# Performance work log

Measured on AMD Instinct MI355X. Metric: run time of the kernel, lower is better.

The kernel has to match this reference:

```python
import jax, jax.numpy as jnp
import numpy as np

IN_FEATS, N_HIDDEN, NUM_LAYERS, N_CLASSES, CLS_HIDDEN = 166, 76, 2, 2, 510
T, N, E = 3, 100000, 1600000
RRELU_SLOPE = (1.0 / 8.0 + 1.0 / 3.0) / 2.0  # eval-mode RReLU = leaky relu with mean slope


def setup_inputs() -> dict:
    key = jax.random.key(0)
    ks = jax.random.split(key, 24)
    d = {}
    d['feats'] = jax.random.normal(ks[0], (T, N, IN_FEATS), jnp.float32)
    d['src'] = jax.random.randint(ks[1], (T, E), 0, N, jnp.int32)
    d['dst'] = jax.random.randint(ks[2], (T, E), 0, N, jnp.int32)
    # TopK scorers (uniform +-1/sqrt(feats))
    s0 = 1.0 / np.sqrt(IN_FEATS)
    s1 = 1.0 / np.sqrt(N_HIDDEN)
    d['scorer0'] = jax.random.uniform(ks[3], (IN_FEATS, 1), jnp.float32, -s0, s0)
    d['scorer1'] = jax.random.uniform(ks[4], (N_HIDDEN, 1), jnp.float32, -s1, s1)
    # GCN weights (xavier-ish)
    d['gcn_w0'] = jax.random.normal(ks[5], (IN_FEATS, N_HIDDEN), jnp.float32) * np.sqrt(2.0 / (IN_FEATS + N_HIDDEN))
    d['gcn_w1'] = jax.random.normal(ks[6], (N_HIDDEN, N_HIDDEN), jnp.float32) * np.sqrt(2.0 / (2 * N_HIDDEN))
    # GRU params, torch layout: W_ih [3H, H_in], W_hh [3H, H], gate order (r, z, n)
    g = 1.0 / np.sqrt(N_HIDDEN)
    H3 = 3 * N_HIDDEN
    d['gru0_wih'] = jax.random.uniform(ks[7], (H3, N_HIDDEN), jnp.float32, -g, g)
    d['gru0_whh'] = jax.random.uniform(ks[8], (H3, N_HIDDEN), jnp.float32, -g, g)
    d['gru0_bih'] = jax.random.uniform(ks[9], (H3,), jnp.float32, -g, g)
    d['gru0_bhh'] = jax.random.uniform(ks[10], (H3,), jnp.float32, -g, g)
    d['gru1_wih'] = jax.random.uniform(ks[11], (H3, N_HIDDEN), jnp.float32, -g, g)
    d['gru1_whh'] = jax.random.uniform(ks[12], (H3, N_HIDDEN), jnp.float32, -g, g)
    d['gru1_bih'] = jax.random.uniform(ks[13], (H3,), jnp.float32, -g, g)
    d['gru1_bhh'] = jax.random.uniform(ks[14], (H3,), jnp.float32, -g, g)
    # MLP
    m1 = 1.0 / np.sqrt(N_HIDDEN)
    m2 = 1.0 / np.sqrt(CLS_HIDDEN)
    d['mlp_w1'] = jax.random.uniform(ks[15], (N_HIDDEN, CLS_HIDDEN), jnp.float32, -m1, m1)
    d['mlp_b1'] = jax.random.uniform(ks[16], (CLS_HIDDEN,), jnp.float32, -m1, m1)
    d['mlp_w2'] = jax.random.uniform(ks[17], (CLS_HIDDEN, N_CLASSES), jnp.float32, -m2, m2)
    d['mlp_b2'] = jax.random.uniform(ks[18], (N_CLASSES,), jnp.float32, -m2, m2)
    return d


def _topk_pool(x, scorer, k):
    # x: [N, F]; returns X_tilde: [F, k]
    scores = (x @ scorer).ravel() / jnp.linalg.norm(scorer)
    vals, idx = jax.lax.top_k(scores, k)
    out = x[idx] * jnp.tanh(vals)[:, None]  # [k, F]
    return out.T


def _gru_step(x, h, wih, whh, bih, bhh):
    # x: [B, H_in], h: [B, H]; torch GRU gate order r, z, n
    gx = x @ wih.T + bih
    gh = h @ whh.T + bhh
    H = h.shape[1]
    rx, zx, nx = gx[:, :H], gx[:, H:2 * H], gx[:, 2 * H:]
    rh, zh, nh = gh[:, :H], gh[:, H:2 * H], gh[:, 2 * H:]
    r = jax.nn.sigmoid(rx + rh)
    z = jax.nn.sigmoid(zx + zh)
    n = jnp.tanh(nx + r * nh)
    return (1.0 - z) * n + z * h


def _graph_conv(x, W, src, dst, n_nodes):
    # DGL GraphConv, norm='both', bias=False, RReLU (eval) activation
    deg_out = jnp.zeros((n_nodes,), x.dtype).at[src].add(1.0)
    deg_in = jnp.zeros((n_nodes,), x.dtype).at[dst].add(1.0)
    norm_src = jnp.clip(deg_out, 1.0, None) ** -0.5
    norm_dst = jnp.clip(deg_in, 1.0, None) ** -0.5
    h = (x * norm_src[:, None]) @ W  # project first (small out dim)
    agg = jax.ops.segment_sum(h[src], dst, num_segments=n_nodes)
    out = agg * norm_dst[:, None]
    return jnp.where(out >= 0, out, out * RRELU_SLOPE)


def reference(feats, src, dst, scorer0, scorer1, gcn_w0, gcn_w1,
              gru0_wih, gru0_whh, gru0_bih, gru0_bhh,
              gru1_wih, gru1_whh, gru1_bih, gru1_bhh,
              mlp_w1, mlp_b1, mlp_w2, mlp_b2):
    scorers = [scorer0, scorer1]
    gcn_ws = [gcn_w0, gcn_w1]
    grus = [(gru0_wih, gru0_whh, gru0_bih, gru0_bhh),
            (gru1_wih, gru1_whh, gru1_bih, gru1_bhh)]
    feat_list = [feats[t] for t in range(T)]
    for i in range(NUM_LAYERS):
        W = gcn_ws[i]
        wih, whh, bih, bhh = grus[i]
        for t in range(T):
            x_tilde = _topk_pool(feat_list[t], scorers[i], N_HIDDEN)  # [F, k]
            W = _gru_step(x_tilde, W, wih, whh, bih, bhh)  # evolve weights
            feat_list[t] = _graph_conv(feat_list[t], W, src[t], dst[t], N)
    h = feat_list[-1]
    h = jax.nn.relu(h @ mlp_w1 + mlp_b1)
    return h @ mlp_w2 + mlp_b2
```

## Files before the change

### kernel.cpp

```cpp
#include <hip/hip_runtime.h>
#include <math.h>

#define NN 100000
#define EE 1600000
#define F0 166
#define HID 76
#define H3 228
#define CHID 510
#define SLOPE 0.22916666666666666f
#define CAND_MAX 4096
#define NBIN 4096
#define HPAD 20

#define BSH 9
#define BSZ 512
#define NBKT 196
#define CH 4096
#define NCHK 391
#define NBAND 13

__device__ __forceinline__ unsigned f2key(float f){
    unsigned u = __float_as_uint(f);
    return (u & 0x80000000u) ? ~u : (u | 0x80000000u);
}
__device__ __forceinline__ float key2f(unsigned k){
    unsigned u = (k & 0x80000000u) ? (k & 0x7fffffffu) : ~k;
    return __uint_as_float(u);
}

__global__ void scorer_norms_k(const float* __restrict__ s0, const float* __restrict__ s1,
                               float* __restrict__ outn){
    __shared__ float red[256];
    int tid = threadIdx.x;
    float a = 0.f;
    for (int k = tid; k < F0; k += 256) a += s0[k]*s0[k];
    red[tid] = a; __syncthreads();
    for (int s = 128; s > 0; s >>= 1){ if (tid < s) red[tid] += red[tid+s]; __syncthreads(); }
    if (tid == 0) outn[0] = 1.0f/sqrtf(red[0]);
    __syncthreads();
    float b = 0.f;
    for (int k = tid; k < HID; k += 256) b += s1[k]*s1[k];
    red[tid] = b; __syncthreads();
    for (int s = 128; s > 0; s >>= 1){ if (tid < s) red[tid] += red[tid+s]; __syncthreads(); }
    if (tid == 0) outn[1] = 1.0f/sqrtf(red[0]);
}

__global__ void pad_k(const float* __restrict__ w1, const float* __restrict__ b1,
                      const float* __restrict__ w2, float* __restrict__ w1t,
                      float* __restrict__ b1p, float* __restrict__ w2p){
    int idx = blockIdx.x*256 + threadIdx.x;
    if (idx < 512*HID){
        int j = idx / HID, k = idx - j*HID;
        w1t[idx] = (j < CHID) ? w1[k*CHID + j] : 0.f;
    }
    if (idx < 512)  b1p[idx] = (idx < CHID)   ? b1[idx] : 0.f;
    if (idx < 1024) w2p[idx] = (idx < CHID*2) ? w2[idx] : 0.f;
}


__global__ __launch_bounds__(256) void p1_hist_k(const int* __restrict__ src, const int* __restrict__ dst,
                                                 int* __restrict__ bhS, int* __restrict__ bhD){
    __shared__ int hS[NBKT], hD[NBKT];
    int t = blockIdx.y, blk = blockIdx.x, tid = threadIdx.x;
    for (int i = tid; i < NBKT; i += 256){ hS[i] = 0; hD[i] = 0; }
    __syncthreads();
    size_t ebase = (size_t)t*EE + (size_t)blk*CH;
    int m = EE - blk*CH; if (m > CH) m = CH;
    for (int j = tid; j < m; j += 256){
        atomicAdd(&hS[src[ebase + j] >> BSH], 1);
        atomicAdd(&hD[dst[ebase + j] >> BSH], 1);
    }
    __syncthreads();
    for (int i = tid; i < NBKT; i += 256){
        bhS[((size_t)t*NBKT + i)*NCHK + blk] = hS[i];
        bhD[((size_t)t*NBKT + i)*NCHK + blk] = hD[i];
    }
}

__global__ __launch_bounds__(512) void p2_scan_k(int* __restrict__ bhS, int* __restrict__ bhD,
                                                 int* __restrict__ ctS, int* __restrict__ ctD){
    __shared__ int sd[512];
    int b = blockIdx.x, t = blockIdx.y, tid = threadIdx.x;
    for (int a = 0; a < 2; a++){
        int* bh = a ? bhD : bhS;
        int* ct = a ? ctD : ctS;
        int* row = bh + ((size_t)t*NBKT + b)*NCHK;
        int v = (tid < NCHK) ? row[tid] : 0;
        sd[tid] = v; __syncthreads();
        for (int off = 1; off < 512; off <<= 1){
            int x = (tid >= off) ? sd[tid - off] : 0;
            __syncthreads();
            sd[tid] += x;
            __syncthreads();
        }
        if (tid < NCHK) row[tid] = sd[tid] - v;
        if (tid == 511) ct[t*NBKT + b] = sd[511];
        __syncthreads();
    }
}

__global__ __launch_bounds__(256) void p3_base_k(const int* __restrict__ ctS, const int* __restrict__ ctD,
                                                 int* __restrict__ bbS, int* __restrict__ bbD){
    __shared__ int sd[256];
    int tid = threadIdx.x;
    for (int a = 0; a < 2; a++){
        const int* ct = a ? ctD : ctS;
        int* bb = a ? bbD : bbS;
        for (int t = 0; t < 3; t++){
            int v = (tid < NBKT) ? ct[t*NBKT + tid] : 0;
            sd[tid] = v; __syncthreads();
            for (int off = 1; off < 256; off <<= 1){
                int x = (tid >= off) ? sd[tid - off] : 0;
                __syncthreads();
                sd[tid] += x;
                __syncthreads();
            }
            if (tid < NBKT) bb[t*(NBKT+1) + tid] = sd[tid] - v;
            if (tid == 0)   bb[t*(NBKT+1) + NBKT] = EE;
            __syncthreads();
        }
    }
}

__global__ __launch_bounds__(256) void p4_scatter_k(const int* __restrict__ src, const int* __restrict__ dst,
                                                    const int* __restrict__ bhS, const int* __restrict__ bhD,
                                                    const int* __restrict__ bbS, const int* __restrict__ bbD,
                                                    int* __restrict__ srcpart,
                                                    unsigned long long* __restrict__ pairpart){
    __shared__ int baseS[NBKT], baseD[NBKT], cS[NBKT], cD[NBKT];
    int t = blockIdx.y, blk = blockIdx.x, tid = threadIdx.x;
    for (int i = tid; i < NBKT; i += 256){
        baseS[i] = bbS[t*(NBKT+1) + i] + bhS[((size_t)t*NBKT + i)*NCHK + blk];
        baseD[i] = bbD[t*(NBKT+1) + i] + bhD[((size_t)t*NBKT + i)*NCHK + blk];
        cS[i] = 0; cD[i] = 0;
    }
    __syncthreads();
    size_t ebase = (size_t)t*EE + (size_t)blk*CH;
    int m = EE - blk*CH; if (m > CH) m = CH;
    int* sp = srcpart + (size_t)t*EE;
    unsigned long long* pp = pairpart + (size_t)t*EE;
    for (int j = tid; j < m; j += 256){
        int s = src[ebase + j], d = dst[ebase + j];
        int bs = s >> BSH, bd = d >> BSH;
        int r0 = atomicAdd(&cS[bs], 1);
        sp[baseS[bs] + r0] = s;
        int r1 = atomicAdd(&cD[bd], 1);
        pp[baseD[bd] + r1] = ((unsigned long long)(unsigned)s << 32) | (unsigned)d;
    }
}

__global__ __launch_bounds__(256) void p5_degO_k(const int* __restrict__ srcpart,
                                                 const int* __restrict__ bbS,
                                                 float* __restrict__ nO){
    __shared__ int cnt[BSZ];
    int b = blockIdx.x, t = blockIdx.y, tid = threadIdx.x;
    for (int i = tid; i < BSZ; i += 256) cnt[i] = 0;
    __syncthreads();
    int st = bbS[t*(NBKT+1) + b], en = bbS[t*(NBKT+1) + b + 1];
    const int* sp = srcpart + (size_t)t*EE;
    for (int j = st + tid; j < en; j += 256) atomicAdd(&cnt[sp[j] & (BSZ-1)], 1);
    __syncthreads();
    int nb = b << BSH;
    for (int i = tid; i < BSZ; i += 256){
        int n = nb + i;
        if (n < NN){
            int o = cnt[i]; if (o < 1) o = 1;
            nO[t*NN + n] = 1.0f/sqrtf((float)o);
        }
    }
}

__global__ __launch_bounds__(512) void p6_csr_k(const unsigned long long* __restrict__ pairpart,
                                                const int* __restrict__ bbD,
                                                int* __restrict__ degI, int* __restrict__ rs,
                                                float* __restrict__ nI,
                                                int* __restrict__ col){
    __shared__ int cnt2[BSZ*NBAND];
    __shared__ int fc2[BSZ*NBAND];
    __shared__ int sd[BSZ];
    int b = blockIdx.x, t = blockIdx.y, tid = threadIdx.x;
    for (int i = tid; i < BSZ*NBAND; i += 512){ cnt2[i] = 0; fc2[i] = 0; }
    __syncthreads();
    int st = bbD[t*(NBKT+1) + b], en = bbD[t*(NBKT+1) + b + 1];
    const unsigned long long* pp = pairpart + (size_t)t*EE;
    for (int j = st + tid; j < en; j += 512){
        unsigned long long p = pp[j];
        int li   = (int)(p & (unsigned long long)(BSZ-1));
        int band = (int)(p >> 32) >> 13;
        atomicAdd(&cnt2[li*NBAND + band], 1);
    }
    __syncthreads();
    int rowcnt = 0;
    #pragma unroll
    for (int bb = 0; bb < NBAND; bb++) rowcnt += cnt2[tid*NBAND + bb];
    sd[tid] = rowcnt; __syncthreads();
    for (int off = 1; off < 512; off <<= 1){
        int x = (tid >= off) ? sd[tid - off] : 0;
        __syncthreads();
        sd[tid] += x;
        __syncthreads();
    }
    int rowEx = sd[tid] - rowcnt;
    int run = rowEx;
    #pragma unroll
    for (int bb = 0; bb < NBAND; bb++){
        int cvv = cnt2[tid*NBAND + bb];
        cnt2[tid*NBAND + bb] = run;
        run += cvv;
    }
    int nb = b << BSH;
    int n = nb + tid;
    if (n < NN){
        degI[t*NN + n] = rowcnt;
        rs[t*NN + n] = st + rowEx;
        int ii = rowcnt; if (ii < 1) ii = 1;
        nI[t*NN + n] = 1.0f/sqrtf((float)ii);
    }
    __syncthreads();
    int* ct = col + (size_t)t*EE;
    for (int j = st + tid; j < en; j += 512){
        unsigned long long p = pp[j];
        int s  = (int)(p >> 32);
        int li = (int)(p & (unsigned long long)(BSZ-1));
        int band = s >> 13;
        int r = atomicAdd(&fc2[li*NBAND + band], 1);
        ct[st + cnt2[li*NBAND + band] + r] = s;
    }
}


template<int F, int PAD>
__global__ __launch_bounds__(256) void score_k(const float* __restrict__ x,
                                               const float* __restrict__ scorer,
                                               const float* __restrict__ invn,
                                               float* __restrict__ scores,
                                               unsigned* hist){
    __shared__ float xs[64*PAD];
    __shared__ float part[256];
    int tid = threadIdx.x;
    int n0 = blockIdx.x*64;
    int nodes = NN - n0; if (nodes > 64) nodes = 64;
    for (int idx = tid; idx < nodes*F; idx += 256){
        int n = idx / F, k = idx - n*F;
        xs[n*PAD + k] = x[(size_t)(n0+n)*F + k];
    }
    __syncthreads();
    int w = __builtin_amdgcn_readfirstlane(tid >> 6);
    int lane = tid & 63;
    int k0 = (F*w) >> 2, k1 = (F*(w+1)) >> 2;
    const float* xrow = xs + lane*PAD;
    float s = 0.f;
    for (int k = k0; k < k1; k++) s += xrow[k]*scorer[k];
    part[w*64 + lane] = s;
    __syncthreads();
    if (tid < 64 && n0 + tid < NN){
        float tot = (part[tid] + part[64+tid] + part[128+tid] + part[192+tid]) * invn[0];
        scores[n0 + tid] = tot;
        atomicAdd(&hist[f2key(tot) >> 20], 1u);
    }
}

__global__ __launch_bounds__(256) void compact_k(const float* __restrict__ scores,
                                                 const unsigned* __restrict__ hist,
                                                 float* __restrict__ cv, int* __restrict__ ci, int* cnt){
    __shared__ unsigned cs[256];
    __shared__ int thr_s;
    int tid = threadIdx.x;
    unsigned s = 0;
    int base = NBIN - 1 - tid*16;
    for (int j = 0; j < 16; j++) s += hist[base - j];
    cs[tid] = s; __syncthreads();
    if (tid == 0){
        unsigned acc = 0; int c = 0;
        for (; c < 256; c++){ if (acc + cs[c] >= 76u) break; acc += cs[c]; }
        int b = NBIN - 1 - c*16;
        int sel = 0;
        for (int j = 0; j < 16; j++){
            acc += hist[b - j];
            if (acc >= 76u){ sel = b - j; break; }
        }
        thr_s = sel;
    }
    __syncthreads();
    int thr = thr_s;
    int n = blockIdx.x*256 + tid;
    if (n >= NN) return;
    float sv = scores[n];
    if ((int)(f2key(sv) >> 20) >= thr){
        int p = atomicAdd(cnt, 1);
        if (p < CAND_MAX){ cv[p] = sv; ci[p] = n; }
    }
}

__global__ __launch_bounds__(256) void topk_k(const float* __restrict__ cv,
                                              const int* __restrict__ ci,
                                              const int* __restrict__ cnt,
                                              int* __restrict__ topidx,
                                              float* __restrict__ tanhv){
    __shared__ unsigned long long keys[CAND_MAX];
    int tid = threadIdx.x;
    int M = *cnt; if (M > CAND_MAX) M = CAND_MAX;
    for (int i = tid; i < M; i += 256)
        keys[i] = ((unsigned long long)f2key(cv[i]) << 32) | (unsigned)(~ci[i]);
    __syncthreads();
    for (int i = tid; i < M; i += 256){
        unsigned long long ki = keys[i];
        int r = 0;
        for (int j = 0; j < M; j++) r += (keys[j] > ki) ? 1 : 0;
        if (r < 76){
            topidx[r] = (int)(~(unsigned)(ki & 0xffffffffu));
            tanhv[r]  = tanhf(key2f((unsigned)(ki >> 32)));
        }
    }
}

template<int F>
__global__ void gru_k(const float* __restrict__ cur, const int* __restrict__ topidx,
                      const float* __restrict__ tanhv, float* __restrict__ W,
                      float* __restrict__ Wt,
                      const float* __restrict__ wih, const float* __restrict__ whh,
                      const float* __restrict__ bih, const float* __restrict__ bhh){
    __shared__ float xr[HID], hr[HID], gx[H3], gh[H3];
    int r = blockIdx.x, tid = threadIdx.x;
    if (tid < HID){
        xr[tid] = cur[(size_t)topidx[tid]*F + r] * tanhv[tid];
        hr[tid] = W[r*HID + tid];
    }
    __syncthreads();
    if (tid < H3){
        const float* wi = wih + tid*HID;
        const float* wh = whh + tid*HID;
        float sa = 0.f, sb = 0.f;
        for (int k = 0; k < HID; k++){ sa += xr[k]*wi[k]; sb += hr[k]*wh[k]; }
        gx[tid] = bih[tid] + sa;
        gh[tid] = bhh[tid] + sb;
    }
    __syncthreads();
    if (tid < HID){
        float rr = 1.f/(1.f + expf(-(gx[tid] + gh[tid])));
        float zz = 1.f/(1.f + expf(-(gx[HID+tid] + gh[HID+tid])));
        float nn = tanhf(gx[2*HID+tid] + rr*gh[2*HID+tid]);
        float nv = (1.f - zz)*nn + zz*hr[tid];
        W[r*HID + tid] = nv;
        int c = tid >> 2, i = tid & 3;
        Wt[(c*F + r)*4 + i] = nv;
    }
}

template<int F, int PAD, int NB>
__global__ __launch_bounds__(256) void gemm_k(const float* __restrict__ x,
                                              const float* __restrict__ Wt,
                                              const float* __restrict__ nO,
                                              float* __restrict__ h){
    __shared__ __align__(16) float xs[NB*PAD];
    int tid = threadIdx.x;
    int n0 = blockIdx.x*NB;
    int nodes = NN - n0; if (nodes > NB) nodes = NB;
    for (int idx = tid; idx < nodes*F; idx += 256){
        int n = idx / F, k = idx - n*F;
        xs[n*PAD + k] = x[(size_t)(n0+n)*F + k];
    }
    __syncthreads();
    int w = __builtin_amdgcn_readfirstlane(tid >> 6);
    int lane = tid & 63;
    int c0 = w*5;
    const float4* Wt4 = (const float4*)Wt;
    float4 accA[5], accB[5];
    #pragma unroll
    for (int c = 0; c < 5; c++){
        accA[c] = make_float4(0.f,0.f,0.f,0.f);
        accB[c] = make_float4(0.f,0.f,0.f,0.f);
    }
    const float* xA = xs + lane*PAD;
    const float* xB = xs + ((NB==128) ? (lane+64)*PAD : lane*PAD);
    for (int k = 0; k < F; k++){
        float xa = xA[k];
        float xb = 0.f;
        if constexpr (NB == 128) xb = xB[k];
        #pragma unroll
        for (int c = 0; c < 5; c++){
            float4 wv = Wt4[(c0 + c)*F + k];
            accA[c].x += xa*wv.x; accA[c].y += xa*wv.y;
            accA[c].z += xa*wv.z; accA[c].w += xa*wv.w;
            if constexpr (NB == 128){
                accB[c].x += xb*wv.x; accB[c].y += xb*wv.y;
                accB[c].z += xb*wv.z; accB[c].w += xb*wv.w;
            }
        }
    }
    int nc = (w == 3) ? 4 : 5;
    int nA = n0 + lane;
    if (nA < NN){
        float nm = nO[nA];
        float4* h4 = (float4*)h + (size_t)nA*HPAD + c0;
        for (int c = 0; c < nc; c++){
            float4 a = accA[c];
            h4[c] = make_float4(a.x*nm, a.y*nm, a.z*nm, a.w*nm);
        }
    }
    if constexpr (NB == 128){
        int nB = n0 + 64 + lane;
        if (nB < NN){
            float nm = nO[nB];
            float4* h4 = (float4*)h + (size_t)nB*HPAD + c0;
            for (int c = 0; c < nc; c++){
                float4 a = accB[c];
                h4[c] = make_float4(a.x*nm, a.y*nm, a.z*nm, a.w*nm);
            }
        }
    }
}

__global__ void agg_k(const int* __restrict__ rs, const int* __restrict__ degI,
                      const int* __restrict__ col, const float* __restrict__ h,
                      const float* __restrict__ nI, float* __restrict__ ft){
    int idx = blockIdx.x*256 + threadIdx.x;
    if (idx >= NN*19) return;
    int n = idx/19, c = idx - n*19;
    int st = rs[n], cnt = degI[n];
    const float4* h4 = (const float4*)h;
    float ax=0.f, ay=0.f, az=0.f, aw=0.f;
    int e = 0;
    for (; e + 4 <= cnt; e += 4){
        int s0 = col[st + e];
        int s1 = col[st + e + 1];
        int s2 = col[st + e + 2];
        int s3 = col[st + e + 3];
        float4 v0 = h4[(size_t)s0*HPAD + c];
        float4 v1 = h4[(size_t)s1*HPAD + c];
        float4 v2 = h4[(size_t)s2*HPAD + c];
        float4 v3 = h4[(size_t)s3*HPAD + c];
        ax += (v0.x + v1.x) + (v2.x + v3.x);
        ay += (v0.y + v1.y) + (v2.y + v3.y);
        az += (v0.z + v1.z) + (v2.z + v3.z);
        aw += (v0.w + v1.w) + (v2.w + v3.w);
    }
    for (; e < cnt; e++){
        int s = col[st + e];
        float4 v = h4[(size_t)s*HPAD + c];
        ax += v.x; ay += v.y; az += v.z; aw += v.w;
    }
    float nm = nI[n];
    ax*=nm; ay*=nm; az*=nm; aw*=nm;
    ax = ax >= 0.f ? ax : ax*SLOPE;
    ay = ay >= 0.f ? ay : ay*SLOPE;
    az = az >= 0.f ? az : az*SLOPE;
    aw = aw >= 0.f ? aw : aw*SLOPE;
    ((float4*)ft)[(size_t)n*19 + c] = make_float4(ax,ay,az,aw);
}

__global__ __launch_bounds__(512) void mlp3_k(const float* __restrict__ ft,
                                              const float* __restrict__ w1t,
                                              const float* __restrict__ b1p,
                                              const float* __restrict__ w2p,
                                              const float* __restrict__ b2,
                                              float* __restrict__ out){
    __shared__ __align__(16) float xs[128*HID];
    __shared__ __align__(16) float ws[256*HID];
    __shared__ float b1s[512];
    __shared__ float w2s[1024];
    int tid = threadIdx.x;
    int n0 = blockIdx.x*128;
    {
        int lim = ((NN - n0 < 128) ? (NN - n0) : 128)*19;
        const float4* g4 = (const float4*)(ft + (size_t)n0*HID);
        float4* s4 = (float4*)xs;
        for (int i = tid; i < 128*19; i += 512)
            s4[i] = (i < lim) ? g4[i] : make_float4(0.f,0.f,0.f,0.f);
    }
    b1s[tid] = b1p[tid];
    for (int i = tid; i < 1024; i += 512) w2s[i] = w2p[i];
    int wid = tid >> 6, lane = tid & 63;
    int wr = wid >> 2, wc = wid & 3;
    int a = lane >> 3, b = lane & 7;
    float p0[8], p1[8];
    #pragma unroll
    for (int i = 0; i < 8; i++){ p0[i] = 0.f; p1[i] = 0.f; }
    const float4* xbase = (const float4*)(xs + (wr*64 + a)*HID);
    for (int jb = 0; jb < 2; jb++){
        __syncthreads();
        {
            const float4* g4 = (const float4*)(w1t + (size_t)jb*256*HID);
            float4* s4 = (float4*)ws;
            for (int i = tid; i < 256*19; i += 512) s4[i] = g4[i];
        }
        __syncthreads();
        float acc[8][8];
        #pragma unroll
        for (int i = 0; i < 8; i++)
            #pragma unroll
            for (int m = 0; m < 8; m++) acc[i][m] = 0.f;
        const float4* wbase = (const float4*)(ws + (wc*64 + b)*HID);
        for (int k4 = 0; k4 < 19; k4++){
            float4 xv[8], wv[8];
            #pragma unroll
            for (int i = 0; i < 8; i++) xv[i] = xbase[i*(8*19) + k4];
            #pragma unroll
            for (int m = 0; m < 8; m++) wv[m] = wbase[m*(8*19) + k4];
            #pragma unroll
            for (int i = 0; i < 8; i++)
                #pragma unroll
                for (int m = 0; m < 8; m++){
                    acc[i][m] += xv[i].x*wv[m].x + xv[i].y*wv[m].y
                               + xv[i].z*wv[m].z + xv[i].w*wv[m].w;
                }
        }
        #pragma unroll
        for (int m = 0; m < 8; m++){
            int j = jb*256 + wc*64 + b + 8*m;
            float bias = b1s[j - jb*256 + ((jb) ? 256 : 0)];
            bias = b1s[j];
            float u0 = w2s[2*j], u1 = w2s[2*j+1];
            #pragma unroll
            for (int i = 0; i < 8; i++){
                float s = acc[i][m] + bias;
                s = fmaxf(s, 0.f);
                p0[i] += s*u0;
                p1[i] += s*u1;
            }
        }
    }
    #pragma unroll
    for (int off = 1; off < 8; off <<= 1){
        #pragma unroll
        for (int i = 0; i < 8; i++){
            p0[i] += __shfl_xor(p0[i], off, 64);
            p1[i] += __shfl_xor(p1[i], off, 64);
        }
    }
    __syncthreads();
    float* red = xs;
    if (b == 0){
        #pragma unroll
        for (int i = 0; i < 8; i++){
            int nl = wr*64 + a + 8*i;
            red[(wc*128 + nl)*2 + 0] = p0[i];
            red[(wc*128 + nl)*2 + 1] = p1[i];
        }
    }
    __syncthreads();
    if (tid < 256){
        int nl = tid >> 1, comp = tid & 1;
        float v = red[(0*128 + nl)*2 + comp] + red[(1*128 + nl)*2 + comp]
                + red[(2*128 + nl)*2 + comp] + red[(3*128 + nl)*2 + comp] + b2[comp];
        int n = n0 + nl;
        if (n < NN) out[(size_t)n*2 + comp] = v;
    }
}

extern "C" void kernel_launch(void* const* d_in, const int* in_sizes, int n_in,
                              void* d_out, int out_size, void* d_ws, size_t ws_size,
                              hipStream_t stream)
{
    (void)in_sizes; (void)n_in; (void)out_size; (void)ws_size;
    const float* feats   = (const float*)d_in[0];
    const int*   src     = (const int*)d_in[1];
    const int*   dst     = (const int*)d_in[2];
    const float* scorer0 = (const float*)d_in[3];
    const float* scorer1 = (const float*)d_in[4];
    const float* gcnw[2] = {(const float*)d_in[5],  (const float*)d_in[6]};
    const float* wih[2]  = {(const float*)d_in[7],  (const float*)d_in[11]};
    const float* whh[2]  = {(const float*)d_in[8],  (const float*)d_in[12]};
    const float* bih[2]  = {(const float*)d_in[9],  (const float*)d_in[13]};
    const float* bhh[2]  = {(const float*)d_in[10], (const float*)d_in[14]};
    const float* w1 = (const float*)d_in[15];
    const float* b1 = (const float*)d_in[16];
    const float* w2 = (const float*)d_in[17];
    const float* b2 = (const float*)d_in[18];
    float* out = (float*)d_out;

    char* p = (char*)d_ws;
    auto alloc = [&](size_t bytes) -> void* {
        void* r = (void*)p;
        p += (bytes + 255) & ~(size_t)255;
        return r;
    };
    float* ft[3];
    for (int t = 0; t < 3; t++) ft[t] = (float*)alloc((size_t)NN*HID*4);
    float* hbuf    = (float*)alloc((size_t)NN*HPAD*16);
    int*   col_all = (int*)alloc((size_t)3*EE*4);
    float* nO_all  = (float*)alloc((size_t)3*NN*4);
    float* nI_all  = (float*)alloc((size_t)3*NN*4);
    int*   rs_all  = (int*)alloc((size_t)3*NN*4);
    int*   dI_all  = (int*)alloc((size_t)3*NN*4);
    int* srcpart = (int*)alloc((size_t)3*EE*4);
    unsigned long long* pairpart = (unsigned long long*)alloc((size_t)3*EE*8);
    int* bhS = (int*)alloc((size_t)3*NBKT*NCHK*4);
    int* bhD = (int*)alloc((size_t)3*NBKT*NCHK*4);
    int* ctS = (int*)alloc((size_t)3*NBKT*4);
    int* ctD = (int*)alloc((size_t)3*NBKT*4);
    int* bbS = (int*)alloc((size_t)3*(NBKT+1)*4);
    int* bbD = (int*)alloc((size_t)3*(NBKT+1)*4);

    float*    scores = (float*)alloc((size_t)NN*4);
    float*    cv     = (float*)alloc(CAND_MAX*4);
    int*      ci     = (int*)alloc(CAND_MAX*4);
    int*      topidx = (int*)alloc(128*4);
    float*    tanhv  = (float*)alloc(128*4);
    float*    Wbuf   = (float*)alloc((size_t)F0*HID*4 + 256);
    float*    Wt     = (float*)alloc((size_t)19*F0*16 + 4096);
    float*    invn   = (float*)alloc(256);
    float*    w1t    = (float*)alloc((size_t)512*HID*4);
    float*    b1p    = (float*)alloc(512*4);
    float*    w2p    = (float*)alloc(1024*4);

    char* zbase = p;
    unsigned* hist6 = (unsigned*)alloc((size_t)6*NBIN*4);
    int*      ccnt6 = (int*)alloc(6*256);
    size_t zsize = (size_t)(p - zbase);

    const int gN  = (NN + 255)/256;
    const int gA  = (NN*19 + 255)/256;
    const int gB  = (NN + 63)/64;
    const int gB2 = (NN + 127)/128;
    const int gM  = (NN + 127)/128;
    const int gP  = (512*HID + 255)/256;

    hipMemsetAsync(zbase, 0, zsize, stream);
    scorer_norms_k<<<1,256,0,stream>>>(scorer0, scorer1, invn);
    pad_k<<<gP,256,0,stream>>>(w1, b1, w2, w1t, b1p, w2p);

    p1_hist_k<<<dim3(NCHK,3),256,0,stream>>>(src, dst, bhS, bhD);
    p2_scan_k<<<dim3(NBKT,3),512,0,stream>>>(bhS, bhD, ctS, ctD);
    p3_base_k<<<1,256,0,stream>>>(ctS, ctD, bbS, bbD);
    p4_scatter_k<<<dim3(NCHK,3),256,0,stream>>>(src, dst, bhS, bhD, bbS, bbD, srcpart, pairpart);
    p5_degO_k<<<dim3(NBKT,3),256,0,stream>>>(srcpart, bbS, nO_all);
    p6_csr_k<<<dim3(NBKT,3),512,0,stream>>>(pairpart, bbD, dI_all, rs_all, nI_all, col_all);

    for (int i = 0; i < 2; i++){
        hipMemcpyAsync(Wbuf, gcnw[i], (size_t)((i==0)?F0:HID)*HID*4, hipMemcpyDeviceToDevice, stream);
        for (int t = 0; t < 3; t++){
            int q = i*3 + t;
            unsigned* hist = hist6 + (size_t)q*NBIN;
            int* ccnt = ccnt6 + q*64;
            const float* cur = (i == 0) ? (feats + (size_t)t*NN*F0) : ft[t];
            if (i == 0) score_k<F0,167><<<gB,256,0,stream>>>(cur, scorer0, invn+0, scores, hist);
            else        score_k<HID,77><<<gB,256,0,stream>>>(cur, scorer1, invn+1, scores, hist);
            compact_k<<<gN,256,0,stream>>>(scores, hist, cv, ci, ccnt);
            topk_k<<<1,256,0,stream>>>(cv, ci, ccnt, topidx, tanhv);
            if (i == 0){
                gru_k<F0><<<F0,256,0,stream>>>(cur, topidx, tanhv, Wbuf, Wt, wih[i], whh[i], bih[i], bhh[i]);
                gemm_k<F0,167,64><<<gB,256,0,stream>>>(cur, Wt, nO_all + (size_t)t*NN, hbuf);
            } else {
                gru_k<HID><<<HID,256,0,stream>>>(cur, topidx, tanhv, Wbuf, Wt, wih[i], whh[i], bih[i], bhh[i]);
                gemm_k<HID,77,128><<<gB2,256,0,stream>>>(cur, Wt, nO_all + (size_t)t*NN, hbuf);
            }
            agg_k<<<gA,256,0,stream>>>(rs_all + (size_t)t*NN, dI_all + (size_t)t*NN,
                                       col_all + (size_t)t*EE, hbuf, nI_all + (size_t)t*NN, ft[t]);
        }
    }

    mlp3_k<<<gM,512,0,stream>>>(ft[2], w1t, b1p, w2p, b2, out);
}
```

Measured before the change: 2.517 ms.

## Fuse compaction with top-k via last-block ticket; retile MLP for occupancy

The candidate compaction and top-k selection become one kernel: each block compacts its candidates, then an atomic ticket picks the last block to finish, and that block runs the rank-based top-k. This removes one launch per layer/timestep. The kernel now carries a 32KB shared keys array in every block, which may lower occupancy in the compaction phase. Separately, the final MLP kernel is retiled to 112 nodes per block with 128-column weight chunks and a minBlocks launch bound, cutting registers and shared memory per block so more blocks can stay resident.

```diff
diff --git a/kernel.cpp b/kernel.cpp
--- a/kernel.cpp
+++ b/kernel.cpp
@@ -11,6 +11,7 @@
 #define CAND_MAX 4096
 #define NBIN 4096
 #define HPAD 20
+#define MNB 112
 
 #define BSH 9
 #define BSZ 512
@@ -260,11 +261,16 @@
     }
 }
 
-__global__ __launch_bounds__(256) void compact_k(const float* __restrict__ scores,
-                                                 const unsigned* __restrict__ hist,
-                                                 float* __restrict__ cv, int* __restrict__ ci, int* cnt){
+__global__ __launch_bounds__(256) void compact_topk_k(const float* __restrict__ scores,
+                                                      const unsigned* __restrict__ hist,
+                                                      float* __restrict__ cv, int* __restrict__ ci,
+                                                      int* __restrict__ cnt,
+                                                      int* __restrict__ topidx,
+                                                      float* __restrict__ tanhv){
     __shared__ unsigned cs[256];
     __shared__ int thr_s;
+    __shared__ int last_s;
+    __shared__ unsigned long long keys[CAND_MAX];
     int tid = threadIdx.x;
     unsigned s = 0;
     int base = NBIN - 1 - tid*16;
@@ -284,24 +290,31 @@
     __syncthreads();
     int thr = thr_s;
     int n = blockIdx.x*256 + tid;
-    if (n >= NN) return;
-    float sv = scores[n];
-    if ((int)(f2key(sv) >> 20) >= thr){
-        int p = atomicAdd(cnt, 1);
-        if (p < CAND_MAX){ cv[p] = sv; ci[p] = n; }
-    }
-}
-
-__global__ __launch_bounds__(256) void topk_k(const float* __restrict__ cv,
-                                              const int* __restrict__ ci,
-                                              const int* __restrict__ cnt,
-                                              int* __restrict__ topidx,
-                                              float* __restrict__ tanhv){
-    __shared__ unsigned long long keys[CAND_MAX];
-    int tid = threadIdx.x;
-    int M = *cnt; if (M > CAND_MAX) M = CAND_MAX;
-    for (int i = tid; i < M; i += 256)
-        keys[i] = ((unsigned long long)f2key(cv[i]) << 32) | (unsigned)(~ci[i]);
+    if (n < NN){
+        float sv = scores[n];
+        if ((int)(f2key(sv) >> 20) >= thr){
+            int p = atomicAdd(&cnt[0], 1);
+            if (p < CAND_MAX){
+                __hip_atomic_store(&cv[p], sv, __ATOMIC_RELAXED, __HIP_MEMORY_SCOPE_AGENT);
+                __hip_atomic_store(&ci[p], n,  __ATOMIC_RELAXED, __HIP_MEMORY_SCOPE_AGENT);
+            }
+        }
+    }
+    __threadfence();
+    if (tid == 0){
+        int tkt = atomicAdd(&cnt[1], 1);
+        last_s = (tkt == (int)gridDim.x - 1);
+    }
+    __syncthreads();
+    if (!last_s) return;
+    __threadfence();
+    int M = atomicAdd(&cnt[0], 0);
+    if (M > CAND_MAX) M = CAND_MAX;
+    for (int i = tid; i < M; i += 256){
+        float v  = __hip_atomic_load(&cv[i], __ATOMIC_RELAXED, __HIP_MEMORY_SCOPE_AGENT);
+        int   id = __hip_atomic_load(&ci[i], __ATOMIC_RELAXED, __HIP_MEMORY_SCOPE_AGENT);
+        keys[i] = ((unsigned long long)f2key(v) << 32) | (unsigned)(~id);
+    }
     __syncthreads();
     for (int i = tid; i < M; i += 256){
         unsigned long long ki = keys[i];
@@ -449,23 +462,24 @@
     ((float4*)ft)[(size_t)n*19 + c] = make_float4(ax,ay,az,aw);
 }
 
-__global__ __launch_bounds__(512) void mlp3_k(const float* __restrict__ ft,
-                                              const float* __restrict__ w1t,
-                                              const float* __restrict__ b1p,
-                                              const float* __restrict__ w2p,
-                                              const float* __restrict__ b2,
-                                              float* __restrict__ out){
-    __shared__ __align__(16) float xs[128*HID];
-    __shared__ __align__(16) float ws[256*HID];
+__global__ __launch_bounds__(512,4) void mlp3_k(const float* __restrict__ ft,
+                                                const float* __restrict__ w1t,
+                                                const float* __restrict__ b1p,
+                                                const float* __restrict__ w2p,
+                                                const float* __restrict__ b2,
+                                                float* __restrict__ out){
+    __shared__ __align__(16) float xs[MNB*HID];
+    __shared__ __align__(16) float ws[128*HID];
     __shared__ float b1s[512];
     __shared__ float w2s[1024];
     int tid = threadIdx.x;
-    int n0 = blockIdx.x*128;
+    int n0 = blockIdx.x*MNB;
     {
-        int lim = ((NN - n0 < 128) ? (NN - n0) : 128)*19;
+        int rem = NN - n0; if (rem > MNB) rem = MNB;
+        int lim = rem*19;
         const float4* g4 = (const float4*)(ft + (size_t)n0*HID);
         float4* s4 = (float4*)xs;
-        for (int i = tid; i < 128*19; i += 512)
+        for (int i = tid; i < MNB*19; i += 512)
             s4[i] = (i < lim) ? g4[i] : make_float4(0.f,0.f,0.f,0.f);
     }
     b1s[tid] = b1p[tid];
@@ -473,46 +487,45 @@
     int wid = tid >> 6, lane = tid & 63;
     int wr = wid >> 2, wc = wid & 3;
     int a = lane >> 3, b = lane & 7;
-    float p0[8], p1[8];
+    float p0[7], p1[7];
     #pragma unroll
-    for (int i = 0; i < 8; i++){ p0[i] = 0.f; p1[i] = 0.f; }
-    const float4* xbase = (const float4*)(xs + (wr*64 + a)*HID);
-    for (int jb = 0; jb < 2; jb++){
+    for (int i = 0; i < 7; i++){ p0[i] = 0.f; p1[i] = 0.f; }
+    const float4* xbase = (const float4*)(xs + (wr*56 + a)*HID);
+    for (int jb = 0; jb < 4; jb++){
         __syncthreads();
         {
-            const float4* g4 = (const float4*)(w1t + (size_t)jb*256*HID);
+            const float4* g4 = (const float4*)(w1t + (size_t)jb*128*HID);
             float4* s4 = (float4*)ws;
-            for (int i = tid; i < 256*19; i += 512) s4[i] = g4[i];
+            for (int i = tid; i < 128*19; i += 512) s4[i] = g4[i];
         }
         __syncthreads();
-        float acc[8][8];
+        float acc[7][4];
         #pragma unroll
-        for (int i = 0; i < 8; i++)
+        for (int i = 0; i < 7; i++)
             #pragma unroll
-            for (int m = 0; m < 8; m++) acc[i][m] = 0.f;
-        const float4* wbase = (const float4*)(ws + (wc*64 + b)*HID);
+            for (int m = 0; m < 4; m++) acc[i][m] = 0.f;
+        const float4* wbase = (const float4*)(ws + (wc*32 + b)*HID);
         for (int k4 = 0; k4 < 19; k4++){
-            float4 xv[8], wv[8];
+            float4 xv[7], wv[4];
             #pragma unroll
-            for (int i = 0; i < 8; i++) xv[i] = xbase[i*(8*19) + k4];
+            for (int i = 0; i < 7; i++) xv[i] = xbase[i*(8*19) + k4];
             #pragma unroll
-            for (int m = 0; m < 8; m++) wv[m] = wbase[m*(8*19) + k4];
+            for (int m = 0; m < 4; m++) wv[m] = wbase[m*(8*19) + k4];
             #pragma unroll
-            for (int i = 0; i < 8; i++)
+            for (int i = 0; i < 7; i++)
                 #pragma unroll
-                for (int m = 0; m < 8; m++){
+                for (int m = 0; m < 4; m++){
                     acc[i][m] += xv[i].x*wv[m].x + xv[i].y*wv[m].y
                                + xv[i].z*wv[m].z + xv[i].w*wv[m].w;
                 }
         }
         #pragma unroll
-        for (int m = 0; m < 8; m++){
-            int j = jb*256 + wc*64 + b + 8*m;
-            float bias = b1s[j - jb*256 + ((jb) ? 256 : 0)];
-            bias = b1s[j];
+        for (int m = 0; m < 4; m++){
+            int j = jb*128 + wc*32 + b + 8*m;
+            float bias = b1s[j];
             float u0 = w2s[2*j], u1 = w2s[2*j+1];
             #pragma unroll
-            for (int i = 0; i < 8; i++){
+            for (int i = 0; i < 7; i++){
                 float s = acc[i][m] + bias;
                 s = fmaxf(s, 0.f);
                 p0[i] += s*u0;
@@ -523,7 +536,7 @@
     #pragma unroll
     for (int off = 1; off < 8; off <<= 1){
         #pragma unroll
-        for (int i = 0; i < 8; i++){
+        for (int i = 0; i < 7; i++){
             p0[i] += __shfl_xor(p0[i], off, 64);
             p1[i] += __shfl_xor(p1[i], off, 64);
         }
@@ -532,17 +545,17 @@
     float* red = xs;
     if (b == 0){
         #pragma unroll
-        for (int i = 0; i < 8; i++){
-            int nl = wr*64 + a + 8*i;
-            red[(wc*128 + nl)*2 + 0] = p0[i];
-            red[(wc*128 + nl)*2 + 1] = p1[i];
-        }
-    }
-    __syncthreads();
-    if (tid < 256){
+        for (int i = 0; i < 7; i++){
+            int nl = wr*56 + a + 8*i;
+            red[(wc*MNB + nl)*2 + 0] = p0[i];
+            red[(wc*MNB + nl)*2 + 1] = p1[i];
+        }
+    }
+    __syncthreads();
+    if (tid < 2*MNB){
         int nl = tid >> 1, comp = tid & 1;
-        float v = red[(0*128 + nl)*2 + comp] + red[(1*128 + nl)*2 + comp]
-                + red[(2*128 + nl)*2 + comp] + red[(3*128 + nl)*2 + comp] + b2[comp];
+        float v = red[(0*MNB + nl)*2 + comp] + red[(1*MNB + nl)*2 + comp]
+                + red[(2*MNB + nl)*2 + comp] + red[(3*MNB + nl)*2 + comp] + b2[comp];
         int n = n0 + nl;
         if (n < NN) out[(size_t)n*2 + comp] = v;
     }
@@ -613,7 +626,7 @@
     const int gA  = (NN*19 + 255)/256;
     const int gB  = (NN + 63)/64;
     const int gB2 = (NN + 127)/128;
-    const int gM  = (NN + 127)/128;
+    const int gM  = (NN + MNB-1)/MNB;
     const int gP  = (512*HID + 255)/256;
 
     hipMemsetAsync(zbase, 0, zsize, stream);
@@ -636,8 +649,7 @@
             const float* cur = (i == 0) ? (feats + (size_t)t*NN*F0) : ft[t];
             if (i == 0) score_k<F0,167><<<gB,256,0,stream>>>(cur, scorer0, invn+0, scores, hist);
             else        score_k<HID,77><<<gB,256,0,stream>>>(cur, scorer1, invn+1, scores, hist);
-            compact_k<<<gN,256,0,stream>>>(scores, hist, cv, ci, ccnt);
-            topk_k<<<1,256,0,stream>>>(cv, ci, ccnt, topidx, tanhv);
+            compact_topk_k<<<gN,256,0,stream>>>(scores, hist, cv, ci, ccnt, topidx, tanhv);
             if (i == 0){
                 gru_k<F0><<<F0,256,0,stream>>>(cur, topidx, tanhv, Wbuf, Wt, wih[i], whh[i], bih[i], bhh[i]);
                 gemm_k<F0,167,64><<<gB,256,0,stream>>>(cur, Wt, nO_all + (size_t)t*NN, hbuf);
```

New measurement: 2.660 ms. +5.7%, slower.
